# Kernel optimization log

Measured on AMD Instinct MI355X. Metric: run time of the kernel, lower is better.

Reference implementation:

```python
import jax, jax.numpy as jnp
import numpy as np

KS = 3        # kernel_size
STRIDE = 1    # patch_stride
RATE = 2      # compression_rate
SCALE = 10.0  # softmax_scale
FUSE_K = 3    # fuse_kernel
EPS = 1e-9
RAW_K = 2 * RATE


def _pad_same(x, k, stride, dilation):
    # TF-style SAME zero padding, matching the torch module's same_pad.
    H, W = x.shape[-2], x.shape[-1]
    oh, ow = -(-H // stride), -(-W // stride)
    eff = (k - 1) * dilation + 1
    ph = max(0, (oh - 1) * stride + eff - H)
    pw = max(0, (ow - 1) * stride + eff - W)
    pads = [(0, 0)] * (x.ndim - 2) + [(ph // 2, ph - ph // 2), (pw // 2, pw - pw // 2)]
    return jnp.pad(x, pads), oh, ow


def extract_patches(x, k, stride, dilation):
    # x: [B,C,H,W] -> [B, L, C, k, k]; L row-major over output grid (== torch Unfold + view/permute)
    xp, oh, ow = _pad_same(x, k, stride, dilation)
    B, C = x.shape[0], x.shape[1]
    cols = [xp[:, :,
               i * dilation: i * dilation + (oh - 1) * stride + 1: stride,
               j * dilation: j * dilation + (ow - 1) * stride + 1: stride]
            for i in range(k) for j in range(k)]
    p = jnp.stack(cols, axis=2).reshape(B, C, k, k, oh * ow)
    return p.transpose(0, 4, 1, 2, 3), oh, ow


def _diag_fuse(x):
    # SAME conv of a 2D map with an eye(FUSE_K) kernel == sum of FUSE_K diagonal shifts.
    pad = FUSE_K - 1
    t = pad // 2
    xp = jnp.pad(x, ((t, pad - t), (t, pad - t)))
    return sum(xp[d:d + x.shape[0], d:d + x.shape[1]] for d in range(FUSE_K))


def _forward(fg, bg, mask):
    B, C, H, W = fg.shape
    # raw (full-res) background patches -> transpose-conv reconstruction weights  [B,L,C,4,4]
    wr, _, _ = extract_patches(bg, RAW_K, RATE * STRIDE, RATE)
    # nearest downsample by RATE (torch F.interpolate nearest, scale 1/RATE)
    fgd = fg[:, :, ::RATE, ::RATE]
    bgd = bg[:, :, ::RATE, ::RATE]
    hd, wd = fgd.shape[2], fgd.shape[3]
    # matching weights from downsampled background  [B,L,C,3,3]
    w, _, _ = extract_patches(bgd, KS, STRIDE, 1)
    # mask resized (nearest) to downsampled grid, patch means  [B,L]
    md = mask[:, :, ::H // hd, ::W // wd]
    mp, _, _ = extract_patches(md, KS, STRIDE, 1)
    m = jnp.mean(mp, axis=(2, 3, 4))
    # foreground patches (SAME, stride 1) for the dynamic-weight conv  [B,Lf,C,3,3]
    fp, _, _ = extract_patches(fgd, KS, 1, 1)

    def per_sample(fp_i, w_i, wr_i, m_i):
        # L2-normalize each background patch (eps added per element, as in torch code)
        norm = jnp.sqrt(jnp.sum(w_i ** 2 + EPS, axis=(1, 2, 3), keepdims=True))
        wn = w_i / norm
        # conv2d(fg, weight) == patch-matching GEMM: sim[l, q] over fg positions q
        sim = jnp.einsum('qcij,lcij->lq', fp_i, wn)  # [L, Lf]
        # fuse: diagonal smoothing along both (bg-patch, fg-pixel) axis pairings
        s = _diag_fuse(sim)
        s = s.reshape(hd, wd, hd, wd).transpose(1, 0, 3, 2).reshape(wd * hd, wd * hd)
        s = _diag_fuse(s)
        sim = s.reshape(wd, hd, wd, hd).transpose(1, 0, 3, 2).reshape(hd * wd, hd, wd)
        mi = m_i[:, None, None]
        sim = jax.nn.softmax(sim * mi * SCALE, axis=0) * mi  # softmax over L
        # conv_transpose2d(sim, wr, stride=RATE) via lhs-dilated conv with flipped kernel
        wk = jnp.flip(wr_i, axis=(2, 3)).transpose(1, 0, 2, 3)  # [C, L, 4, 4]
        y = jax.lax.conv_general_dilated(
            sim[None], wk, window_strides=(1, 1),
            padding=[(RAW_K - 1, RAW_K - 1)] * 2,
            lhs_dilation=(RATE, RATE),
            dimension_numbers=('NCHW', 'OIHW', 'NCHW'))
        return y[0, :, :H, :W] / float(RAW_K ** 2)

    return jax.vmap(per_sample)(fp, w, wr, m)  # [B, C, H, W]


def setup_inputs() -> dict:
    key = jax.random.key(0)
    k1, k2, k3 = jax.random.split(key, 3)
    B, C, H, W = 4, 96, 96, 96
    fg = jax.random.normal(k1, (B, C, H, W), dtype=jnp.float32)
    bg = jax.random.normal(k2, (B, C, H, W), dtype=jnp.float32)
    mask = jnp.round(jax.random.uniform(k3, (B, 1, H, W), dtype=jnp.float32))
    return {"fg": fg, "bg": bg, "mask": mask}


def reference(fg, bg, mask):
    return _forward(fg, bg, mask)
```

## Files before the change

kernel.cpp:

```cpp
#include <hip/hip_runtime.h>
#include <hip/hip_bf16.h>
#include <cstdint>

#define ND 48
#define LQ 2304
#define CCH 96
#define HWD 96
#define CHW (CCH*HWD*HWD)
#define HW2 (HWD*HWD)
#define K2P 2560
#define NJ2 384
#define KSP 384

typedef __attribute__((ext_vector_type(8))) short bf16x8;
typedef __attribute__((ext_vector_type(4))) float f32x4;

__device__ __forceinline__ float4 ld4u(const float* p) {
  float4 v; __builtin_memcpy(&v, p, 16); return v;
}

__global__ void k_down(const float* __restrict__ fg, const float* __restrict__ bg,
                       float* __restrict__ fgdT, float* __restrict__ bgdT,
                       float* __restrict__ n2, size_t sd, size_t sp) {
  int b = blockIdx.z;
  const float* fgb = fg + (size_t)b * CHW;
  const float* bgb = bg + (size_t)b * CHW;
  float* fT = fgdT + (size_t)b * sd;
  float* bT = bgdT + (size_t)b * sd;
  float* n2b = n2 + (size_t)b * sp;
  int p = blockIdx.x * 256 + threadIdx.x;
  if (p >= LQ) return;
  int py = p / ND, px = p % ND;
  const float* fsrc = fgb + (2 * py) * HWD + 2 * px;
  const float* gsrc = bgb + (2 * py) * HWD + 2 * px;
  float s = 0.f;
  for (int c = 0; c < CCH; ++c) {
    float f = fsrc[c * HW2];
    float g = gsrc[c * HW2];
    fT[c * LQ + p] = f;
    bT[c * LQ + p] = g;
    s += g * g;
  }
  n2b[p] = s;
}

__global__ void k_aux(const float* __restrict__ n2, const float* __restrict__ mask,
                      float* __restrict__ rnorm, float* __restrict__ mval, size_t sp) {
  int b = blockIdx.z;
  const float* n2b = n2 + (size_t)b * sp;
  const float* mb = mask + (size_t)b * HW2;
  float* rn = rnorm + (size_t)b * sp;
  float* mv = mval + (size_t)b * sp;
  int p = blockIdx.x * 256 + threadIdx.x;
  if (p >= LQ) return;
  int py = p / ND, px = p % ND;
  float ssq = 0.f, ms = 0.f;
  for (int dy = -1; dy <= 1; ++dy)
    for (int dx = -1; dx <= 1; ++dx) {
      int yy = py + dy, xx = px + dx;
      if (yy >= 0 && yy < ND && xx >= 0 && xx < ND) {
        ssq += n2b[yy * ND + xx];
        ms  += mb[(2 * yy) * HWD + 2 * xx];
      }
    }
  rn[p] = 1.0f / sqrtf(ssq + 864.0f * 1e-9f);
  mv[p] = ms * (1.0f / 9.0f);
}

__global__ __launch_bounds__(256) void k_split(const float* __restrict__ fgdT,
                                               const float* __restrict__ bgdT,
                                               __hip_bfloat16* __restrict__ AB,
                                               size_t sd, size_t sAB) {
  int b = blockIdx.z;
  const float* fT = fgdT + (size_t)b * sd;
  const float* gT = bgdT + (size_t)b * sd;
  __hip_bfloat16* Ao = AB + (size_t)b * sAB;
  __hip_bfloat16* Bo = Ao + (size_t)LQ * KSP;
  __shared__ float fs[96 * 65], gs[96 * 65];
  int q0 = blockIdx.x * 64;
  int tid = threadIdx.x;
#pragma unroll
  for (int i = 0; i < 24; ++i) {
    int e = i * 256 + tid;
    int c = e >> 6, qq = e & 63;
    fs[c * 65 + qq] = fT[c * LQ + q0 + qq];
    gs[c * 65 + qq] = gT[c * LQ + q0 + qq];
  }
  __syncthreads();
  for (int i = 0; i < 24; ++i) {
    int e = i * 256 + tid;
    int qq = e / 96, k4 = (e % 96) * 4;
    unsigned short a4[4], b4[4];
    if (k4 < 288) {
      int part = k4 / 96, c = k4 % 96;
#pragma unroll
      for (int j = 0; j < 4; ++j) {
        float f = fs[(c + j) * 65 + qq];
        float g = gs[(c + j) * 65 + qq];
        __hip_bfloat16 fh = __float2bfloat16(f);
        __hip_bfloat16 gh = __float2bfloat16(g);
        __hip_bfloat16 fl = __float2bfloat16(f - __bfloat162float(fh));
        __hip_bfloat16 gl = __float2bfloat16(g - __bfloat162float(gh));
        __hip_bfloat16 av = (part == 2) ? fl : fh;
        __hip_bfloat16 bv = (part == 1) ? gl : gh;
        a4[j] = *(unsigned short*)&av;
        b4[j] = *(unsigned short*)&bv;
      }
    } else {
      a4[0] = a4[1] = a4[2] = a4[3] = 0;
      b4[0] = b4[1] = b4[2] = b4[3] = 0;
    }
    __builtin_memcpy(&Ao[(size_t)(q0 + qq) * KSP + k4], a4, 8);
    __builtin_memcpy(&Bo[(size_t)(q0 + qq) * KSP + k4], b4, 8);
  }
}

__device__ __forceinline__ void gload16(const void* g, void* l) {
  __builtin_amdgcn_global_load_lds((const __attribute__((address_space(1))) void*)g,
                                   (__attribute__((address_space(3))) void*)l, 16, 0, 0);
}

__global__ __launch_bounds__(256) void k_rgemm_mfma(const __hip_bfloat16* __restrict__ AB,
                                                    float* __restrict__ R,
                                                    size_t sAB, size_t sR) {
  int bz = blockIdx.z;
  const __hip_bfloat16* Aq = AB + (size_t)bz * sAB;
  const __hip_bfloat16* Bq = Aq + (size_t)LQ * KSP;
  float* Rb = R + (size_t)bz * sR;
  __shared__ __align__(16) __hip_bfloat16 As[2][64 * 128];
  __shared__ __align__(16) __hip_bfloat16 Bs[2][64 * 128];
  int m0 = blockIdx.y * 64, n0 = blockIdx.x * 64;
  int tid = threadIdx.x;
  int w = tid >> 6, lane = tid & 63;
  int wm = w >> 1, wn = w & 1;
  f32x4 acc[2][2] = {};

  auto STAGE = [&](int buf, int k0) {
#pragma unroll
    for (int i = 0; i < 4; ++i) {
      int g = i * 256 + tid;
      int row = g >> 4, slot = g & 15;
      int ks = 8 * (slot ^ (row & 7));
      gload16(Aq + (size_t)(m0 + row) * KSP + k0 + ks, &As[buf][g * 8]);
      gload16(Bq + (size_t)(n0 + row) * KSP + k0 + ks, &Bs[buf][g * 8]);
    }
  };

  STAGE(0, 0);
  __syncthreads();
  int cur = 0;
  for (int t = 0; t < 3; ++t) {
    if (t + 1 < 3) STAGE(cur ^ 1, (t + 1) * 128);
#pragma unroll
    for (int kk = 0; kk < 128; kk += 32) {
      bf16x8 af[2], bfr[2];
#pragma unroll
      for (int mi = 0; mi < 2; ++mi) {
        int row = wm * 32 + mi * 16 + (lane & 15);
        int e = (kk + (lane >> 4) * 8) ^ ((row & 7) * 8);
        af[mi] = *(const bf16x8*)(&As[cur][row * 128 + e]);
      }
#pragma unroll
      for (int ni = 0; ni < 2; ++ni) {
        int row = wn * 32 + ni * 16 + (lane & 15);
        int e = (kk + (lane >> 4) * 8) ^ ((row & 7) * 8);
        bfr[ni] = *(const bf16x8*)(&Bs[cur][row * 128 + e]);
      }
#pragma unroll
      for (int mi = 0; mi < 2; ++mi)
#pragma unroll
        for (int ni = 0; ni < 2; ++ni)
          acc[mi][ni] = __builtin_amdgcn_mfma_f32_16x16x32_bf16(af[mi], bfr[ni], acc[mi][ni], 0, 0, 0);
    }
    __syncthreads();
    cur ^= 1;
  }

#pragma unroll
  for (int mi = 0; mi < 2; ++mi)
#pragma unroll
    for (int ni = 0; ni < 2; ++ni)
#pragma unroll
      for (int rr = 0; rr < 4; ++rr) {
        int row = m0 + wm * 32 + mi * 16 + (lane >> 4) * 4 + rr;
        int col = n0 + wn * 32 + ni * 16 + (lane & 15);
        Rb[(size_t)row * LQ + col] = acc[mi][ni][rr];
      }
}

__global__ void k_t9v(const float* __restrict__ R, const float* __restrict__ rnorm,
                      float* __restrict__ A2, size_t sR, size_t sp) {
  int b = blockIdx.z;
  const float* S = R + (size_t)b * sR;
  const float* rn = rnorm + (size_t)b * sp;
  float* O = A2 + (size_t)b * sR;
  int bid = blockIdx.x;
  int wg = (bid & 7) * 648 + (bid >> 3);
  int t = wg * 256 + threadIdx.x;
  int id = t * 4;
  int q = id / LQ, l = id % LQ;
  int qy = q / ND, qx = q % ND;
  int ly = l / ND, lx0 = l % ND;
  float4 acc = make_float4(0.f, 0.f, 0.f, 0.f);
#pragma unroll
  for (int dy = -1; dy <= 1; ++dy) {
    if (qy + dy < 0 || qy + dy >= ND || ly + dy < 0 || ly + dy >= ND) continue;
#pragma unroll
    for (int dx = -1; dx <= 1; ++dx) {
      if (qx + dx < 0 || qx + dx >= ND) continue;
      int off = (dy * ND + dx) * (LQ + 1);
      float4 m = ld4u(S + id + off);
      if (dx == -1 && lx0 == 0) m.x = 0.f;
      if (dx == 1 && lx0 == ND - 4) m.w = 0.f;
      acc.x += m.x; acc.y += m.y; acc.z += m.z; acc.w += m.w;
    }
  }
  float4 r4 = *(const float4*)(rn + l);
  acc.x *= r4.x; acc.y *= r4.y; acc.z *= r4.z; acc.w *= r4.w;
  *(float4*)(O + id) = acc;
}

__global__ void k_fusev(const float* __restrict__ A2, float* __restrict__ F, size_t sR) {
  int b = blockIdx.z;
  const float* S = A2 + (size_t)b * sR;
  float* Fo = F + (size_t)b * sR;
  int bid = blockIdx.x;
  int wg = (bid & 7) * 648 + (bid >> 3);
  int t = wg * 256 + threadIdx.x;
  int id = t * 4;
  int a = id / LQ, bc0 = id % LQ;
  float4 c = *(const float4*)(S + id);
  if (a > 0) {
    float4 m = ld4u(S + id - LQ - 1);
    if (bc0 == 0) m.x = 0.f;
    c.x += m.x; c.y += m.y; c.z += m.z; c.w += m.w;
  }
  if (a < LQ - 1) {
    float4 p = ld4u(S + id + LQ + 1);
    if (bc0 == LQ - 4) p.w = 0.f;
    c.x += p.x; c.y += p.y; c.z += p.z; c.w += p.w;
  }
  *(float4*)(Fo + id) = c;
}

__global__ __launch_bounds__(256) void k_softmax(const float* __restrict__ F,
                                                 const float* __restrict__ mval,
                                                 __hip_bfloat16* __restrict__ P50s,
                                                 size_t sR, size_t sp, size_t sP) {
  int b = blockIdx.z;
  const float* Fb = F + (size_t)b * sR;
  const float* mv = mval + (size_t)b * sp;
  __hip_bfloat16* Pb = P50s + (size_t)b * sP + K2P;
  int q = blockIdx.x;
  int qy = q / ND, qx = q % ND;
  int tid = threadIdx.x;
  __shared__ float red[256];
  int gqv[3]; bool qok[3];
#pragma unroll
  for (int t = 0; t < 3; ++t) {
    int fq = qx * ND + qy + (t - 1);
    qok[t] = (fq >= 0 && fq < LQ);
    gqv[t] = qok[t] ? (fq % ND) * ND + fq / ND : 0;
  }
  float logit[9];
  float vmax = -1e30f;
#pragma unroll
  for (int s = 0; s < 9; ++s) {
    int l = tid + s * 256;
    int ly = l / ND, lx = l % ND;
    float v = 0.f;
#pragma unroll
    for (int t = 0; t < 3; ++t) {
      if (!qok[t]) continue;
      int fl = lx * ND + ly + (t - 1);
      if (fl < 0 || fl >= LQ) continue;
      int gl = (fl % ND) * ND + fl / ND;
      v += Fb[(size_t)gqv[t] * LQ + gl];
    }
    float lg = v * (10.0f * mv[l]);
    logit[s] = lg;
    vmax = fmaxf(vmax, lg);
  }
  red[tid] = vmax;
  __syncthreads();
  for (int w = 128; w > 0; w >>= 1) {
    if (tid < w) red[tid] = fmaxf(red[tid], red[tid + w]);
    __syncthreads();
  }
  float m = red[0];
  __syncthreads();
  float e[9], ssum = 0.f;
#pragma unroll
  for (int s = 0; s < 9; ++s) { e[s] = __expf(logit[s] - m); ssum += e[s]; }
  red[tid] = ssum;
  __syncthreads();
  for (int w = 128; w > 0; w >>= 1) {
    if (tid < w) red[tid] += red[tid + w];
    __syncthreads();
  }
  float inv = 1.0f / red[0];
  __hip_bfloat16 z = __float2bfloat16(0.f);
#pragma unroll
  for (int s = 0; s < 9; ++s) {
    int l = tid + s * 256;
    float p = e[s] * inv * mv[l];
    int col = (l / ND) * 50 + (l % ND);
    Pb[(size_t)q * K2P + col] = __float2bfloat16(p);
  }
  int pc;
  if (tid < 96)        pc = (tid >> 1) * 50 + ND + (tid & 1);
  else if (tid < 196)  pc = 2400 + (tid - 96);
  else                 pc = 2500 + (tid - 196);
  Pb[(size_t)q * K2P + pc] = z;
  if (q == 0)
    for (int i = tid; i < K2P; i += 256) (Pb - K2P)[i] = z;
}

__global__ void k_q2v(const __hip_bfloat16* __restrict__ P50s,
                      __hip_bfloat16* __restrict__ Q2, size_t sP, size_t sQ) {
  int bz = blockIdx.z;
  const __hip_bfloat16* P = P50s + (size_t)bz * sP + K2P;
  __hip_bfloat16* Q = Q2 + (size_t)bz * sQ;
  int bid = blockIdx.x;
  int wg = (bid & 7) * 360 + (bid >> 3);
  int id = wg * 256 + threadIdx.x;
  int r = id / 320, c8 = (id % 320) * 8;
  int a = r / ND, b = r % ND;
  const __hip_bfloat16* base = P + (size_t)r * K2P + c8;
  float acc[8];
  {
    unsigned short s[8]; __builtin_memcpy(s, base, 16);
#pragma unroll
    for (int i = 0; i < 8; ++i) {
      unsigned int u = ((unsigned int)s[i]) << 16;
      acc[i] = __builtin_bit_cast(float, u);
    }
  }
  if (b >= 1) {
    unsigned short s[8]; __builtin_memcpy(s, base - (K2P + 2), 16);
#pragma unroll
    for (int i = 0; i < 8; ++i) {
      unsigned int u = ((unsigned int)s[i]) << 16;
      acc[i] += __builtin_bit_cast(float, u);
    }
  }
  if (a >= 1) {
    unsigned short s[8]; __builtin_memcpy(s, base - (ND * K2P + 100), 16);
#pragma unroll
    for (int i = 0; i < 8; ++i) {
      unsigned int u = ((unsigned int)s[i]) << 16;
      acc[i] += __builtin_bit_cast(float, u);
    }
  }
  if (a >= 1 && b >= 1) {
    unsigned short s[8]; __builtin_memcpy(s, base - ((ND + 1) * K2P + 102), 16);
#pragma unroll
    for (int i = 0; i < 8; ++i) {
      unsigned int u = ((unsigned int)s[i]) << 16;
      acc[i] += __builtin_bit_cast(float, u);
    }
  }
  __hip_bfloat16 o[8];
#pragma unroll
  for (int i = 0; i < 8; ++i) o[i] = __float2bfloat16(acc[i]);
  *(bf16x8*)(Q + (size_t)r * K2P + c8) = *(bf16x8*)o;
}

__global__ void k_b2(const float* __restrict__ bgdT, __hip_bfloat16* __restrict__ B2,
                     size_t sd, size_t sB) {
  int b = blockIdx.z;
  const float* gT = bgdT + (size_t)b * sd;
  __hip_bfloat16* Bb = B2 + (size_t)b * sB;
  int id = blockIdx.x * 256 + threadIdx.x;
  if (id >= NJ2 * K2P) return;
  int j = id / K2P, col = id % K2P;
  int c = j >> 2, s = (j >> 1) & 1, t = j & 1;
  float v = 0.f;
  if (col < 2500) {
    int m = col / 50, n = col % 50;
    int ry = m + s - 1, rx = n + t - 1;
    if (ry >= 0 && ry < ND && rx >= 0 && rx < ND)
      v = gT[c * LQ + ry * ND + rx];
  }
  Bb[id] = __float2bfloat16(v);
}

__global__ __launch_bounds__(256) void k_gemm3(const __hip_bfloat16* __restrict__ A,
                                               const __hip_bfloat16* __restrict__ B,
                                               float* __restrict__ out,
                                               size_t sQ, size_t sB) {
  int bz = blockIdx.z;
  const __hip_bfloat16* Ab = A + (size_t)bz * sQ;
  const __hip_bfloat16* Bb = B + (size_t)bz * sB;
  float* ob = out + (size_t)bz * CHW;
  int wg = (blockIdx.x & 7) * 27 + (blockIdx.x >> 3);
  int n0 = (wg % 6) * 64, m0 = (wg / 6) * 64;
  __shared__ __align__(16) __hip_bfloat16 As[2][64 * 64];
  __shared__ __align__(16) __hip_bfloat16 Bs[2][64 * 64];
  int tid = threadIdx.x;
  int w = tid >> 6, lane = tid & 63;
  int wm = w >> 1, wn = w & 1;
  int l3 = lane >> 3, l7 = lane & 7;
  int kswz = (l7 * 8) ^ (l3 << 3);
  f32x4 acc[2][2] = {};

  auto STAGE = [&](int buf, int k0) {
#pragma unroll
    for (int i = 0; i < 2; ++i) {
      int chunk = w * 2 + i;
      int row = chunk * 8 + l3;
      gload16(Ab + (size_t)(m0 + row) * K2P + k0 + kswz, &As[buf][chunk * 8 * 64]);
      gload16(Bb + (size_t)(n0 + row) * K2P + k0 + kswz, &Bs[buf][chunk * 8 * 64]);
    }
  };

  STAGE(0, 0);
  __syncthreads();
  int cur = 0;
  constexpr int NT = K2P / 64;
  for (int t = 0; t < NT; ++t) {
    if (t + 1 < NT) STAGE(cur ^ 1, (t + 1) * 64);
#pragma unroll
    for (int kk = 0; kk < 64; kk += 32) {
      bf16x8 af[2], bfr[2];
#pragma unroll
      for (int mi = 0; mi < 2; ++mi) {
        int row = wm * 32 + mi * 16 + (lane & 15);
        int e = (kk + (lane >> 4) * 8) ^ ((row & 7) * 8);
        af[mi] = *(const bf16x8*)(&As[cur][row * 64 + e]);
      }
#pragma unroll
      for (int ni = 0; ni < 2; ++ni) {
        int row = wn * 32 + ni * 16 + (lane & 15);
        int e = (kk + (lane >> 4) * 8) ^ ((row & 7) * 8);
        bfr[ni] = *(const bf16x8*)(&Bs[cur][row * 64 + e]);
      }
#pragma unroll
      for (int mi = 0; mi < 2; ++mi)
#pragma unroll
        for (int ni = 0; ni < 2; ++ni)
          acc[mi][ni] = __builtin_amdgcn_mfma_f32_16x16x32_bf16(af[mi], bfr[ni], acc[mi][ni], 0, 0, 0);
    }
    __syncthreads();
    cur ^= 1;
  }

#pragma unroll
  for (int mi = 0; mi < 2; ++mi)
#pragma unroll
    for (int ni = 0; ni < 2; ++ni)
#pragma unroll
      for (int rr = 0; rr < 4; ++rr) {
        int r_ = m0 + wm * 32 + mi * 16 + (lane >> 4) * 4 + rr;
        int j  = n0 + wn * 32 + ni * 16 + (lane & 15);
        int a = r_ / ND, bcol = r_ % ND;
        int c = j >> 2, s = (j >> 1) & 1, tt = j & 1;
        ob[((size_t)c * HWD + 2 * a + s) * HWD + 2 * bcol + tt] = acc[mi][ni][rr] * 0.0625f;
      }
}

extern "C" void kernel_launch(void* const* d_in, const int* in_sizes, int n_in,
                              void* d_out, int out_size, void* d_ws, size_t ws_size,
                              hipStream_t stream) {
  const float* fg_all = (const float*)d_in[0];
  const float* bg_all = (const float*)d_in[1];
  const float* mask_all = (const float*)d_in[2];
  float* out_all = (float*)d_out;
  float* ws = (float*)d_ws;

  int B = in_sizes[0] / CHW;

  const size_t S_D = (size_t)CCH * LQ;
  const size_t S_P = LQ;
  const size_t S_R = (size_t)LQ * LQ;
  const size_t S_P50 = (size_t)(LQ + 1) * K2P;
  const size_t per_floats = S_D * 2 + S_P * 3 + S_R * 2 + S_P50 / 2;

  bool batched = ws_size >= (size_t)B * per_floats * 4;
  int na = batched ? B : 1;
  int nb = na;

  float* fgdT  = ws;
  float* bgdT  = fgdT + (size_t)na * S_D;
  float* n2    = bgdT + (size_t)na * S_D;
  float* rnorm = n2 + (size_t)na * S_P;
  float* mval  = rnorm + (size_t)na * S_P;
  float* bufA  = mval + (size_t)na * S_P;
  float* bufB  = bufA + (size_t)na * S_R;
  __hip_bfloat16* P50 = (__hip_bfloat16*)(bufB + (size_t)na * S_R);
  __hip_bfloat16* Q2  = (__hip_bfloat16*)bufA;
  __hip_bfloat16* B2  = (__hip_bfloat16*)bufB;
  __hip_bfloat16* ABs = P50;

  size_t sd = batched ? S_D : 0, sp = batched ? S_P : 0, sR = batched ? S_R : 0;
  size_t sP = batched ? S_P50 : 0;
  size_t sQ = batched ? S_R * 2 : 0;
  size_t sB = batched ? S_R * 2 : 0;

  for (int b0 = 0; b0 < B; b0 += nb) {
    const float* fg = fg_all + (size_t)(batched ? 0 : b0) * CHW;
    const float* bg = bg_all + (size_t)(batched ? 0 : b0) * CHW;
    const float* mask = mask_all + (size_t)(batched ? 0 : b0) * HW2;
    float* out = out_all + (size_t)(batched ? 0 : b0) * CHW;

    hipLaunchKernelGGL(k_down, dim3(9, 1, nb), dim3(256), 0, stream,
                       fg, bg, fgdT, bgdT, n2, sd, sp);
    hipLaunchKernelGGL(k_aux, dim3(9, 1, nb), dim3(256), 0, stream,
                       n2, mask, rnorm, mval, sp);
    hipLaunchKernelGGL(k_split, dim3(36, 1, nb), dim3(256), 0, stream,
                       fgdT, bgdT, ABs, sd, sP);
    hipLaunchKernelGGL(k_rgemm_mfma, dim3(36, 36, nb), dim3(256), 0, stream,
                       ABs, bufA, sP, sR);
    hipLaunchKernelGGL(k_t9v, dim3(5184, 1, nb), dim3(256), 0, stream,
                       bufA, rnorm, bufB, sR, sp);
    hipLaunchKernelGGL(k_fusev, dim3(5184, 1, nb), dim3(256), 0, stream,
                       bufB, bufA, sR);
    hipLaunchKernelGGL(k_softmax, dim3(2304, 1, nb), dim3(256), 0, stream,
                       bufA, mval, P50, sR, sp, sP);
    hipLaunchKernelGGL(k_q2v, dim3(2880, 1, nb), dim3(256), 0, stream,
                       P50, Q2, sP, sQ);
    hipLaunchKernelGGL(k_b2, dim3(3840, 1, nb), dim3(256), 0, stream,
                       bgdT, B2, sd, sB);
    hipLaunchKernelGGL(k_gemm3, dim3(216, 1, nb), dim3(256), 0, stream,
                       Q2, B2, out, sQ, sB);
  }
}
```

Measured before the change: 263.1 us.

## Simplify softmax gather indexing, use wave-shuffle reductions, and swizzle block order

```diff
diff --git a/kernel.cpp b/kernel.cpp
--- a/kernel.cpp
+++ b/kernel.cpp
@@ -251,67 +251,72 @@
   const float* Fb = F + (size_t)b * sR;
   const float* mv = mval + (size_t)b * sp;
   __hip_bfloat16* Pb = P50s + (size_t)b * sP + K2P;
-  int q = blockIdx.x;
+  int bid = blockIdx.x;
+  int q = (bid & 7) * 288 + (bid >> 3);
   int qy = q / ND, qx = q % ND;
   int tid = threadIdx.x;
-  __shared__ float red[256];
-  int gqv[3]; bool qok[3];
-#pragma unroll
-  for (int t = 0; t < 3; ++t) {
-    int fq = qx * ND + qy + (t - 1);
-    qok[t] = (fq >= 0 && fq < LQ);
-    gqv[t] = qok[t] ? (fq % ND) * ND + fq / ND : 0;
-  }
-  float logit[9];
+  __shared__ float wred[8];
+  int fq0 = qx * ND + qy - 1, fq2 = qx * ND + qy + 1;
+  bool qok0 = (fq0 >= 0), qok2 = (fq2 < LQ);
+  const float* pm = Fb + (size_t)(qok0 ? ((fq0 % ND) * ND + fq0 / ND) : 0) * LQ;
+  const float* pc = Fb + (size_t)q * LQ;
+  const float* pp = Fb + (size_t)(qok2 ? ((fq2 % ND) * ND + fq2 / ND) : 0) * LQ;
+
+  float logit[9], mvv[9];
   float vmax = -1e30f;
+  int ly = tid / ND, lx = tid % ND;
 #pragma unroll
   for (int s = 0; s < 9; ++s) {
-    int l = tid + s * 256;
-    int ly = l / ND, lx = l % ND;
+    int l = s * 256 + tid;
     float v = 0.f;
-#pragma unroll
-    for (int t = 0; t < 3; ++t) {
-      if (!qok[t]) continue;
-      int fl = lx * ND + ly + (t - 1);
-      if (fl < 0 || fl >= LQ) continue;
-      int gl = (fl % ND) * ND + fl / ND;
-      v += Fb[(size_t)gqv[t] * LQ + gl];
-    }
-    float lg = v * (10.0f * mv[l]);
+    if (qok0) {
+      int off = (ly > 0) ? (l - ND) : (2255 + lx);
+      float val = pm[off];
+      if (ly == 0 && lx == 0) val = 0.f;
+      v += val;
+    }
+    v += pc[l];
+    if (qok2) {
+      int off = (ly < ND - 1) ? (l + ND) : (lx + 1);
+      float val = pp[off];
+      if (ly == ND - 1 && lx == ND - 1) val = 0.f;
+      v += val;
+    }
+    float m = mv[l];
+    mvv[s] = m;
+    float lg = v * (10.0f * m);
     logit[s] = lg;
     vmax = fmaxf(vmax, lg);
-  }
-  red[tid] = vmax;
+    lx += 16; ly += 5; if (lx >= ND) { lx -= ND; ly += 1; }
+  }
+#pragma unroll
+  for (int d = 32; d; d >>= 1) vmax = fmaxf(vmax, __shfl_xor(vmax, d));
+  int wv = tid >> 6, lane = tid & 63;
+  if (lane == 0) wred[wv] = vmax;
   __syncthreads();
-  for (int w = 128; w > 0; w >>= 1) {
-    if (tid < w) red[tid] = fmaxf(red[tid], red[tid + w]);
-    __syncthreads();
-  }
-  float m = red[0];
+  vmax = fmaxf(fmaxf(wred[0], wred[1]), fmaxf(wred[2], wred[3]));
+  float ssum = 0.f;
+#pragma unroll
+  for (int s = 0; s < 9; ++s) { logit[s] = __expf(logit[s] - vmax); ssum += logit[s]; }
+#pragma unroll
+  for (int d = 32; d; d >>= 1) ssum += __shfl_xor(ssum, d);
+  if (lane == 0) wred[4 + wv] = ssum;
   __syncthreads();
-  float e[9], ssum = 0.f;
-#pragma unroll
-  for (int s = 0; s < 9; ++s) { e[s] = __expf(logit[s] - m); ssum += e[s]; }
-  red[tid] = ssum;
-  __syncthreads();
-  for (int w = 128; w > 0; w >>= 1) {
-    if (tid < w) red[tid] += red[tid + w];
-    __syncthreads();
-  }
-  float inv = 1.0f / red[0];
+  float inv = 1.0f / (wred[4] + wred[5] + wred[6] + wred[7]);
+  ly = tid / ND;
+#pragma unroll
+  for (int s = 0; s < 9; ++s) {
+    int l = s * 256 + tid;
+    float p = logit[s] * inv * mvv[s];
+    Pb[(size_t)q * K2P + l + 2 * ly] = __float2bfloat16(p);
+    ly = (s * 256 + 256 + tid) / ND;
+  }
   __hip_bfloat16 z = __float2bfloat16(0.f);
-#pragma unroll
-  for (int s = 0; s < 9; ++s) {
-    int l = tid + s * 256;
-    float p = e[s] * inv * mv[l];
-    int col = (l / ND) * 50 + (l % ND);
-    Pb[(size_t)q * K2P + col] = __float2bfloat16(p);
-  }
-  int pc;
-  if (tid < 96)        pc = (tid >> 1) * 50 + ND + (tid & 1);
-  else if (tid < 196)  pc = 2400 + (tid - 96);
-  else                 pc = 2500 + (tid - 196);
-  Pb[(size_t)q * K2P + pc] = z;
+  int pc2;
+  if (tid < 96)        pc2 = (tid >> 1) * 50 + ND + (tid & 1);
+  else if (tid < 196)  pc2 = 2400 + (tid - 96);
+  else                 pc2 = 2500 + (tid - 196);
+  Pb[(size_t)q * K2P + pc2] = z;
   if (q == 0)
     for (int i = tid; i < K2P; i += 256) (Pb - K2P)[i] = z;
 }
```

New measurement: 253.5 us. 1.04x faster.
